# Optimization experiments

Measured on AMD Instinct MI355X. Metric: run time of the kernel, lower is better.

Reference implementation:

```python
import jax, jax.numpy as jnp
import numpy as np
from jax.scipy.special import erf

N = 128          # n_points
STEPS = 64       # number of velocity steps
MAX_TIME = 100.0
E = 4096         # number of events
P = 4000         # number of unique node pairs
DELTA = MAX_TIME / (STEPS - 1)  # time_delta_size
EPS = 1e-9


def setup_inputs() -> dict:
    key = jax.random.key(0)
    k1, k2, k3 = jax.random.split(key, 3)
    beta = jnp.ones((1, 1), jnp.float32)
    z0 = jax.random.uniform(k1, (N, 2), jnp.float32) * 0.5
    v0 = jax.random.uniform(k2, (N, 2, STEPS), jnp.float32) * 0.5
    # event times strictly inside [0, max_time) so floor(t/DELTA) < STEPS
    event_times = jax.random.uniform(k3, (E,), jnp.float32, 0.0, MAX_TIME * 0.999)
    # unique upper-triangular node pairs (torch.unique on data[:,0:2] hoisted to setup)
    rng = np.random.default_rng(0)
    iu, ju = np.triu_indices(N, k=1)
    sel = rng.choice(iu.shape[0], size=P, replace=False)
    pairs_i = jnp.asarray(iu[sel], jnp.int32)
    pairs_j = jnp.asarray(ju[sel], jnp.int32)
    t0 = jnp.zeros((1,), jnp.float32)
    tn = jnp.full((1,), MAX_TIME, jnp.float32)
    return {"beta": beta, "z0": z0, "v0": v0, "event_times": event_times,
            "t0": t0, "tn": tn, "pairs_i": pairs_i, "pairs_j": pairs_j}


def reference(beta, z0, v0, event_times, t0, tn, pairs_i, pairs_j):
    dtype = z0.dtype
    # time_deltas = cat([0], diff(linspace(0, max_time, steps)))  -> (STEPS,)
    time_deltas = jnp.concatenate(
        [jnp.zeros((1,), dtype), jnp.full((STEPS - 1,), DELTA, dtype)])
    b = beta[0, 0]

    # steps(): per-step starting positions  Z_steps[n, c, s] = z0 + v0 * dt_s
    Z_steps = z0[:, :, None] + v0 * time_deltas              # (N, 2, STEPS)

    # gather time-step latents for each event time
    tv = event_times / DELTA                                 # (E,)
    tf = jnp.floor(tv)
    frac = tv - tf                                           # fractional step offset
    idx = jnp.clip(tf.astype(jnp.int32), 0, STEPS - 1)       # (E,)
    Zt = Z_steps[:, :, idx] + v0[:, :, idx] * frac           # (N, 2, E)

    # event term: sum over unique pairs of (beta - ||z_i(t) - z_j(t)||^2)
    Zi = Zt[pairs_i]                                         # (P, 2, E)
    Zj = Zt[pairs_j]
    d_pairs = jnp.sum((Zi - Zj) ** 2, axis=1)                # (P, E)
    event_intensity = jnp.sum(b - d_pairs)

    # non-event term: analytical integral of exp(beta - ||dz + dv*u||^2)
    # over each step duration, summed over steps, upper triangle only
    dz = Z_steps[:, None] - Z_steps[None, :]                 # (N, N, 2, STEPS)
    dv = v0[:, None] - v0[None, :]                           # (N, N, 2, STEPS)
    r2 = jnp.sum(dv * dv, axis=2) + EPS                      # (N, N, STEPS)
    r = jnp.sqrt(r2)
    zdv = jnp.sum(dz * dv, axis=2)
    bshift = zdv / r2
    c = jnp.sum(dz * dz, axis=2) - zdv * zdv / r2
    integ = (jnp.exp(b - c) * (jnp.sqrt(jnp.pi) / (2.0 * r))
             * (erf(r * (time_deltas + bshift)) - erf(r * bshift)))  # (N,N,STEPS)
    mat = jnp.sum(integ, axis=2)                             # (N, N)
    mask = jnp.triu(jnp.ones((N, N), bool), k=1)
    non_event_intensity = jnp.sum(jnp.where(mask, mat, jnp.zeros((), dtype)))

    return event_intensity - non_event_intensity
```

## Files before the change

kernel.cpp:

```cpp
#include <hip/hip_runtime.h>

#define NPTS   128
#define NSTEPS 64
#define NEV    4096
#define NPAIR  4000
#define DELTA_F (100.0f / 63.0f)
#define EPSF    1e-9f
#define SQRTPI_OVER2 0.88622692545275801365f

#define GRID 256
#define BLK  256
#define POISON 0xAAAAAAAAu


__device__ __forceinline__ void store_agent(float* p, float v) {
    __hip_atomic_store((unsigned int*)p, __builtin_bit_cast(unsigned int, v),
                       __ATOMIC_RELAXED, __HIP_MEMORY_SCOPE_AGENT);
}
__device__ __forceinline__ unsigned int load_agent(const float* p) {
    return __hip_atomic_load((const unsigned int*)p, __ATOMIC_RELAXED,
                             __HIP_MEMORY_SCOPE_AGENT);
}

__global__ __launch_bounds__(BLK) void fused_all(
    const float* __restrict__ beta,
    const float* __restrict__ z0,
    const float* __restrict__ v0,
    const float* __restrict__ event_times,
    const int*   __restrict__ pi,
    const int*   __restrict__ pj,
    float* __restrict__ partials,
    float* __restrict__ out) {
    __shared__ float s1[NSTEPS], s2[NSTEPS];
    __shared__ float zsh[NPTS * 2];
    const int t = threadIdx.x;
    const int bid = blockIdx.x;

    if (t < NSTEPS) { s1[t] = 0.f; s2[t] = 0.f; }
    zsh[t] = z0[t];
    __syncthreads();
    for (int e = t; e < NEV; e += BLK) {
        float tv = event_times[e] / DELTA_F;
        float tf = floorf(tv);
        float f  = tv - tf;
        int s = (int)tf;
        s = s < 0 ? 0 : (s > NSTEPS - 1 ? NSTEPS - 1 : s);
        float a = (s == 0 ? 0.f : DELTA_F) + f;
        atomicAdd(&s1[s], a);
        atomicAdd(&s2[s], a * a);
    }
    __syncthreads();

    const float b = beta[0];

    float lev = 0.f;
    for (int idx = bid * BLK + t; idx < NPAIR * NSTEPS; idx += GRID * BLK) {
        int s = idx & (NSTEPS - 1);
        int p = idx >> 6;
        int i = pi[p], j = pj[p];
        float dz0x = zsh[i * 2 + 0] - zsh[j * 2 + 0];
        float dz0y = zsh[i * 2 + 1] - zsh[j * 2 + 1];
        float dvx = v0[(i * 2 + 0) * NSTEPS + s] - v0[(j * 2 + 0) * NSTEPS + s];
        float dvy = v0[(i * 2 + 1) * NSTEPS + s] - v0[(j * 2 + 1) * NSTEPS + s];
        float Q1 = dz0x * dvx + dz0y * dvy;
        float Q2 = dvx * dvx + dvy * dvy;
        float term = 2.f * s1[s] * Q1 + s2[s] * Q2;
        if (s == 0) term += (float)NEV * (dz0x * dz0x + dz0y * dz0y);
        lev += term;
    }

    float lne = 0.f;
    for (int idx = bid * BLK + t; idx < NPTS * NPTS * NSTEPS; idx += GRID * BLK) {
        int s  = idx & (NSTEPS - 1);
        int ij = idx >> 6;
        int i  = ij >> 7;
        int j  = ij & (NPTS - 1);
        if (j > i) {
            float td = (s == 0) ? 0.f : DELTA_F;
            float dvx = v0[(i * 2 + 0) * NSTEPS + s] - v0[(j * 2 + 0) * NSTEPS + s];
            float dvy = v0[(i * 2 + 1) * NSTEPS + s] - v0[(j * 2 + 1) * NSTEPS + s];
            float dzx = (zsh[i * 2 + 0] - zsh[j * 2 + 0]) + dvx * td;
            float dzy = (zsh[i * 2 + 1] - zsh[j * 2 + 1]) + dvy * td;
            float r2  = dvx * dvx + dvy * dvy + EPSF;
            float r   = sqrtf(r2);
            float zdv = dzx * dvx + dzy * dvy;
            float bsh = zdv / r2;
            float cc  = dzx * dzx + dzy * dzy - zdv * zdv / r2;
            lne += expf(b - cc) * (SQRTPI_OVER2 / r) *
                   (erff(r * (td + bsh)) - erff(r * bsh));
        }
    }

    #pragma unroll
    for (int off = 32; off > 0; off >>= 1) {
        lev += __shfl_down(lev, off, 64);
        lne += __shfl_down(lne, off, 64);
    }
    __shared__ float wsv[4], wsn[4];
    int lane = t & 63, wid = t >> 6;
    if (lane == 0) { wsv[wid] = lev; wsn[wid] = lne; }
    __syncthreads();
    if (t == 0) {
        store_agent(&partials[bid],        wsv[0] + wsv[1] + wsv[2] + wsv[3]);
        store_agent(&partials[GRID + bid], wsn[0] + wsn[1] + wsn[2] + wsn[3]);
    }

    if (bid == 0 && t < 64) {
        for (;;) {
            bool ok = true;
            for (int k = t; k < 2 * GRID; k += 64) {
                if (load_agent(&partials[k]) == POISON) ok = false;
            }
            if (__all(ok)) break;
            __builtin_amdgcn_s_sleep(8);
        }
        double ev = 0.0, ne = 0.0;
        for (int k = t; k < GRID; k += 64) {
            ev += (double)__builtin_bit_cast(float, load_agent(&partials[k]));
            ne += (double)__builtin_bit_cast(float, load_agent(&partials[GRID + k]));
        }
        #pragma unroll
        for (int off = 32; off > 0; off >>= 1) {
            ev += __shfl_down(ev, off, 64);
            ne += __shfl_down(ne, off, 64);
        }
        if (t == 0) {
            double evt = (double)b * (double)NPAIR * (double)NEV - ev;
            out[0] = (float)(evt - ne);
        }
    }
}

extern "C" void kernel_launch(void* const* d_in, const int* in_sizes, int n_in,
                              void* d_out, int out_size, void* d_ws, size_t ws_size,
                              hipStream_t stream) {
    const float* beta        = (const float*)d_in[0];
    const float* z0          = (const float*)d_in[1];
    const float* v0          = (const float*)d_in[2];
    const float* event_times = (const float*)d_in[3];
    const int* pairs_i = (const int*)d_in[6];
    const int* pairs_j = (const int*)d_in[7];
    float* out = (float*)d_out;
    float* partials = (float*)d_ws;

    fused_all<<<GRID, BLK, 0, stream>>>(beta, z0, v0, event_times,
                                        pairs_i, pairs_j, partials, out);
}
```

Measured before the change: 90.03 us.

## Iterate only upper-triangle pairs and compute event histogram once in block 0

The non-event loop now maps one wave to each upper-triangular (i,j) pair, decoding the index with a sqrt, so the half of the N×N grid that was previously masked out is never visited. The s=0 step, whose integral is zero, is dropped through the lane select. The event-time histogram is built only by block 0 and published to workspace, and the other blocks spin-wait on a poison sentinel before the event term, which needs them. This removes the redundant per-block histogram and divergent masked work, but adds a grid-wide dependency on block 0 and relies on the workspace being poison-initialised.

```diff
diff --git a/kernel.cpp b/kernel.cpp
--- a/kernel.cpp
+++ b/kernel.cpp
@@ -4,12 +4,14 @@
 #define NSTEPS 64
 #define NEV    4096
 #define NPAIR  4000
+#define NTRI   (NPTS * (NPTS - 1) / 2)
 #define DELTA_F (100.0f / 63.0f)
 #define EPSF    1e-9f
 #define SQRTPI_OVER2 0.88622692545275801365f
 
 #define GRID 256
 #define BLK  256
+#define NWAVES (GRID * (BLK / 64))
 #define POISON 0xAAAAAAAAu
 
 
@@ -29,66 +31,94 @@
     const float* __restrict__ event_times,
     const int*   __restrict__ pi,
     const int*   __restrict__ pj,
-    float* __restrict__ partials,
+    float* __restrict__ ws,
     float* __restrict__ out) {
+    __shared__ float zsh[NPTS * 2];
     __shared__ float s1[NSTEPS], s2[NSTEPS];
-    __shared__ float zsh[NPTS * 2];
-    const int t = threadIdx.x;
-    const int bid = blockIdx.x;
+    const int t    = threadIdx.x;
+    const int bid  = blockIdx.x;
+    const int lane = t & 63;
+    const int wid  = t >> 6;
 
-    if (t < NSTEPS) { s1[t] = 0.f; s2[t] = 0.f; }
+    float* partials = ws;
+    float* S1g = ws + 512;
+    float* S2g = ws + 576;
+
     zsh[t] = z0[t];
-    __syncthreads();
-    for (int e = t; e < NEV; e += BLK) {
-        float tv = event_times[e] / DELTA_F;
-        float tf = floorf(tv);
-        float f  = tv - tf;
-        int s = (int)tf;
-        s = s < 0 ? 0 : (s > NSTEPS - 1 ? NSTEPS - 1 : s);
-        float a = (s == 0 ? 0.f : DELTA_F) + f;
-        atomicAdd(&s1[s], a);
-        atomicAdd(&s2[s], a * a);
+    const float b = beta[0];
+
+    float a1 = 0.f, a2 = 0.f;
+
+    if (bid == 0) {
+        if (t < NSTEPS) { s1[t] = 0.f; s2[t] = 0.f; }
+        __syncthreads();
+        for (int e = t; e < NEV; e += BLK) {
+            float tv = event_times[e] / DELTA_F;
+            float tf = floorf(tv);
+            float f  = tv - tf;
+            int s = (int)tf;
+            s = s < 0 ? 0 : (s > NSTEPS - 1 ? NSTEPS - 1 : s);
+            float a = (s == 0 ? 0.f : DELTA_F) + f;
+            atomicAdd(&s1[s], a);
+            atomicAdd(&s2[s], a * a);
+        }
+        __syncthreads();
+        if (t < NSTEPS) {
+            store_agent(&S1g[t], s1[t]);
+            store_agent(&S2g[t], s2[t]);
+        }
+        a1 = s1[lane];
+        a2 = s2[lane];
+    } else {
+        __syncthreads();
     }
-    __syncthreads();
 
-    const float b = beta[0];
+    float lne = 0.f;
+    const int wave = bid * (BLK / 64) + wid;
+    for (int r = wave; r < NTRI; r += NWAVES) {
+        double sq = sqrt((double)(65025 - 8 * r));
+        int i = (int)((255.0 - sq) * 0.5);
+        while ((i + 1) * (255 - (i + 1)) / 2 <= r) ++i;
+        while (i * (255 - i) / 2 > r) --i;
+        int j = i + 1 + (r - i * (255 - i) / 2);
+
+        const int s = lane;
+        float dvx = v0[(i * 2 + 0) * NSTEPS + s] - v0[(j * 2 + 0) * NSTEPS + s];
+        float dvy = v0[(i * 2 + 1) * NSTEPS + s] - v0[(j * 2 + 1) * NSTEPS + s];
+        float dzx = (zsh[i * 2 + 0] - zsh[j * 2 + 0]) + dvx * DELTA_F;
+        float dzy = (zsh[i * 2 + 1] - zsh[j * 2 + 1]) + dvy * DELTA_F;
+        float r2  = dvx * dvx + dvy * dvy + EPSF;
+        float rr  = sqrtf(r2);
+        float zdv = dzx * dvx + dzy * dvy;
+        float bsh = zdv / r2;
+        float cc  = dzx * dzx + dzy * dzy - zdv * zdv / r2;
+        float integ = expf(b - cc) * (SQRTPI_OVER2 / rr) *
+                      (erff(rr * (DELTA_F + bsh)) - erff(rr * bsh));
+        lne += (s != 0) ? integ : 0.f;
+    }
+
+    if (bid != 0) {
+        unsigned int u1, u2;
+        do { u1 = load_agent(&S1g[lane]); } while (u1 == POISON);
+        do { u2 = load_agent(&S2g[lane]); } while (u2 == POISON);
+        a1 = __builtin_bit_cast(float, u1);
+        a2 = __builtin_bit_cast(float, u2);
+    }
 
     float lev = 0.f;
     for (int idx = bid * BLK + t; idx < NPAIR * NSTEPS; idx += GRID * BLK) {
-        int s = idx & (NSTEPS - 1);
-        int p = idx >> 6;
+        int p = __builtin_amdgcn_readfirstlane(idx >> 6);
         int i = pi[p], j = pj[p];
+        const int s = lane;
         float dz0x = zsh[i * 2 + 0] - zsh[j * 2 + 0];
         float dz0y = zsh[i * 2 + 1] - zsh[j * 2 + 1];
         float dvx = v0[(i * 2 + 0) * NSTEPS + s] - v0[(j * 2 + 0) * NSTEPS + s];
         float dvy = v0[(i * 2 + 1) * NSTEPS + s] - v0[(j * 2 + 1) * NSTEPS + s];
         float Q1 = dz0x * dvx + dz0y * dvy;
         float Q2 = dvx * dvx + dvy * dvy;
-        float term = 2.f * s1[s] * Q1 + s2[s] * Q2;
+        float term = 2.f * a1 * Q1 + a2 * Q2;
         if (s == 0) term += (float)NEV * (dz0x * dz0x + dz0y * dz0y);
         lev += term;
-    }
-
-    float lne = 0.f;
-    for (int idx = bid * BLK + t; idx < NPTS * NPTS * NSTEPS; idx += GRID * BLK) {
-        int s  = idx & (NSTEPS - 1);
-        int ij = idx >> 6;
-        int i  = ij >> 7;
-        int j  = ij & (NPTS - 1);
-        if (j > i) {
-            float td = (s == 0) ? 0.f : DELTA_F;
-            float dvx = v0[(i * 2 + 0) * NSTEPS + s] - v0[(j * 2 + 0) * NSTEPS + s];
-            float dvy = v0[(i * 2 + 1) * NSTEPS + s] - v0[(j * 2 + 1) * NSTEPS + s];
-            float dzx = (zsh[i * 2 + 0] - zsh[j * 2 + 0]) + dvx * td;
-            float dzy = (zsh[i * 2 + 1] - zsh[j * 2 + 1]) + dvy * td;
-            float r2  = dvx * dvx + dvy * dvy + EPSF;
-            float r   = sqrtf(r2);
-            float zdv = dzx * dvx + dzy * dvy;
-            float bsh = zdv / r2;
-            float cc  = dzx * dzx + dzy * dzy - zdv * zdv / r2;
-            lne += expf(b - cc) * (SQRTPI_OVER2 / r) *
-                   (erff(r * (td + bsh)) - erff(r * bsh));
-        }
     }
 
     #pragma unroll
@@ -97,7 +127,6 @@
         lne += __shfl_down(lne, off, 64);
     }
     __shared__ float wsv[4], wsn[4];
-    int lane = t & 63, wid = t >> 6;
     if (lane == 0) { wsv[wid] = lev; wsn[wid] = lne; }
     __syncthreads();
     if (t == 0) {
@@ -141,8 +170,8 @@
     const int* pairs_i = (const int*)d_in[6];
     const int* pairs_j = (const int*)d_in[7];
     float* out = (float*)d_out;
-    float* partials = (float*)d_ws;
+    float* ws  = (float*)d_ws;
 
     fused_all<<<GRID, BLK, 0, stream>>>(beta, z0, v0, event_times,
-                                        pairs_i, pairs_j, partials, out);
+                                        pairs_i, pairs_j, ws, out);
 }
```

Result: no change. 88.82 us (-1.3%).
